# Kernel optimization log

Measured on AMD Instinct MI355X. Metric: run time of the kernel, lower is better.

Reference implementation:

```python
import jax, jax.numpy as jnp
import numpy as np

D_MODEL = 256
N_HEADS = 8
D_FFN = 1024
B, N = 4, 1024
HEAD_DIM = D_MODEL // N_HEADS
LN_EPS = 1e-5


def _ln(x, g, b):
    mu = jnp.mean(x, axis=-1, keepdims=True)
    var = jnp.var(x, axis=-1, keepdims=True)
    return (x - mu) * jax.lax.rsqrt(var + LN_EPS) * g + b


def setup_inputs() -> dict:
    key = jax.random.key(0)
    ks = jax.random.split(key, 16)
    s = 0.02
    return {
        "embed": jax.random.normal(ks[0], (B, N, D_MODEL), jnp.float32),
        "refer_bbox": jax.random.uniform(ks[1], (B, N, 4), jnp.float32),
        "dist": jax.random.uniform(ks[2], (B, N, N), jnp.float32),
        "query_pos": jax.random.normal(ks[3], (B, N, D_MODEL), jnp.float32),
        "in_proj_w": jax.random.normal(ks[4], (3 * D_MODEL, D_MODEL), jnp.float32) * s,
        "in_proj_b": jnp.zeros((3 * D_MODEL,), jnp.float32),
        "out_w": jax.random.normal(ks[5], (D_MODEL, D_MODEL), jnp.float32) * s,
        "out_b": jnp.zeros((D_MODEL,), jnp.float32),
        "tau_w": jax.random.normal(ks[6], (N_HEADS, D_MODEL), jnp.float32) * s,
        "tau_b": jax.random.uniform(ks[7], (N_HEADS,), jnp.float32, 0.0, 2.0),
        "w1": jax.random.normal(ks[8], (D_FFN, D_MODEL), jnp.float32) * s,
        "b1": jnp.zeros((D_FFN,), jnp.float32),
        "w2": jax.random.normal(ks[9], (D_MODEL, D_FFN), jnp.float32) * s,
        "b2": jnp.zeros((D_MODEL,), jnp.float32),
        "g1": jnp.ones((D_MODEL,), jnp.float32),
        "beta1": jnp.zeros((D_MODEL,), jnp.float32),
        "g2": jnp.ones((D_MODEL,), jnp.float32),
        "beta2": jnp.zeros((D_MODEL,), jnp.float32),
    }


def reference(embed, refer_bbox, dist, query_pos, in_proj_w, in_proj_b, out_w, out_b,
              tau_w, tau_b, w1, b1, w2, b2, g1, beta1, g2, beta2):
    # tau: (B, N, H) -> (B, H, N); additive bias mask[b,h,i,j] = dist[b,i,j] * tau[b,h,i]
    tau = (embed @ tau_w.T + tau_b).transpose(0, 2, 1)
    bias = dist[:, None, :, :] * tau[..., None]  # (B, H, N, N)

    qk = embed + query_pos  # q = k = embed + pos, v = embed
    wq, wk, wv = jnp.split(in_proj_w, 3, axis=0)
    bq, bk, bv = jnp.split(in_proj_b, 3, axis=0)
    q = (qk @ wq.T + bq).reshape(B, N, N_HEADS, HEAD_DIM)
    k = (qk @ wk.T + bk).reshape(B, N, N_HEADS, HEAD_DIM)
    v = (embed @ wv.T + bv).reshape(B, N, N_HEADS, HEAD_DIM)

    scores = jnp.einsum("bihd,bjhd->bhij", q, k) / np.sqrt(HEAD_DIM) + bias
    attn = jax.nn.softmax(scores, axis=-1)
    ctx = jnp.einsum("bhij,bjhd->bihd", attn, v).reshape(B, N, D_MODEL)
    tgt = ctx @ out_w.T + out_b

    x = _ln(embed + tgt, g1, beta1)
    ffn = jax.nn.relu(x @ w1.T + b1) @ w2.T + b2
    return _ln(x + ffn, g2, beta2)
```

## Files before the change

### kernel.cpp

```cpp
#include <hip/hip_runtime.h>
#include <math.h>

#define D_MODEL 256
#define N_HEADS 8
#define HEAD_DIM 32
#define D_FFN   1024
#define BB      4
#define NN      1024
#define M_TOT   (BB * NN)
#define LN_EPS  1e-5f

#define QSCALE_LOG2E 0.2550348612f
#define LOG2E        1.4426950408889634f

typedef float f32x4 __attribute__((ext_vector_type(4)));
typedef short bf16x8 __attribute__((ext_vector_type(8)));

__device__ __forceinline__ unsigned short f2bf(float f) {
    unsigned int u = __float_as_uint(f);
    unsigned int r = (u + 0x7fffu + ((u >> 16) & 1u)) >> 16;
    return (unsigned short)r;
}
__device__ __forceinline__ ushort4 pack4(float4 v) {
    ushort4 o; o.x = f2bf(v.x); o.y = f2bf(v.y); o.z = f2bf(v.z); o.w = f2bf(v.w);
    return o;
}
__device__ __forceinline__ float fast_exp2(float x) {
#if __has_builtin(__builtin_amdgcn_exp2f)
    return __builtin_amdgcn_exp2f(x);
#else
    return exp2f(x);
#endif
}

__global__ __launch_bounds__(256)
void prep_all_kernel(const float4* __restrict__ e, const float4* __restrict__ qp,
                     ushort4* __restrict__ ebf, ushort4* __restrict__ qkbf,
                     const float4* __restrict__ inw, const float4* __restrict__ outw,
                     const float4* __restrict__ w1, const float4* __restrict__ w2,
                     const float4* __restrict__ tauw,
                     ushort4* __restrict__ o_inw, ushort4* __restrict__ o_outw,
                     ushort4* __restrict__ o_w1, ushort4* __restrict__ o_w2,
                     ushort4* __restrict__ o_taupad) {
    if (blockIdx.x < 1024) {
        int i = blockIdx.x * 256 + threadIdx.x;
        float4 ev = e[i], pv = qp[i];
        ebf[i] = pack4(ev);
        float4 s = make_float4(ev.x + pv.x, ev.y + pv.y, ev.z + pv.z, ev.w + pv.w);
        qkbf[i] = pack4(s);
    } else {
        int i = (blockIdx.x - 1024) * 256 + threadIdx.x;
        if (i < 49152)       o_inw[i] = pack4(inw[i]);
        else if (i < 65536)  o_outw[i - 49152] = pack4(outw[i - 49152]);
        else if (i < 131072) o_w1[i - 65536] = pack4(w1[i - 65536]);
        else if (i < 196608) o_w2[i - 131072] = pack4(w2[i - 131072]);
        else if (i < 200704) {
            int q = i - 196608;
            if (q < 512) o_taupad[q] = pack4(tauw[q]);
            else { ushort4 z = {0, 0, 0, 0}; o_taupad[q] = z; }
        }
    }
}

__global__ __launch_bounds__(256)
void qkv_mfma_kernel(const unsigned short* __restrict__ qk_bf,
                     const unsigned short* __restrict__ emb_bf,
                     const unsigned short* __restrict__ inw_bf,
                     const unsigned short* __restrict__ taupad,
                     const float* __restrict__ in_proj_b, const float* __restrict__ tau_b,
                     unsigned short* __restrict__ qb, unsigned short* __restrict__ kb,
                     unsigned short* __restrict__ vbT, float* __restrict__ taub) {
    const int w    = threadIdx.x >> 6;
    const int lane = threadIdx.x & 63;
    const int l16 = lane & 15, l4 = lane >> 4;
    const int n0 = blockIdx.x * 64;
    const int m0 = blockIdx.y * 64;
    const int wm = (w >> 1) * 32, wn = (w & 1) * 32;

    const unsigned short* A = (blockIdx.x < 8) ? qk_bf : emb_bf;
    const unsigned short* W0 = (n0 < 768) ? &inw_bf[(size_t)(n0 + wn + l16) * D_MODEL]
                                          : &taupad[(size_t)(wn + l16) * D_MODEL];
    const unsigned short* Ar0 = &A[(size_t)(m0 + wm + l16) * D_MODEL];

    f32x4 acc[2][2] = {};
    #pragma unroll
    for (int k0 = 0; k0 < D_MODEL; k0 += 32) {
        bf16x8 a0 = *(const bf16x8*)&Ar0[k0 + l4 * 8];
        bf16x8 a1 = *(const bf16x8*)&Ar0[16 * D_MODEL + k0 + l4 * 8];
        bf16x8 b0 = *(const bf16x8*)&W0[k0 + l4 * 8];
        bf16x8 b1 = *(const bf16x8*)&W0[16 * D_MODEL + k0 + l4 * 8];
        acc[0][0] = __builtin_amdgcn_mfma_f32_16x16x32_bf16(a0, b0, acc[0][0], 0, 0, 0);
        acc[0][1] = __builtin_amdgcn_mfma_f32_16x16x32_bf16(a0, b1, acc[0][1], 0, 0, 0);
        acc[1][0] = __builtin_amdgcn_mfma_f32_16x16x32_bf16(a1, b0, acc[1][0], 0, 0, 0);
        acc[1][1] = __builtin_amdgcn_mfma_f32_16x16x32_bf16(a1, b1, acc[1][1], 0, 0, 0);
    }

    #pragma unroll
    for (int i = 0; i < 2; i++) {
        #pragma unroll
        for (int j = 0; j < 2; j++) {
            #pragma unroll
            for (int r = 0; r < 4; r++) {
                const int m = m0 + wm + i * 16 + l4 * 4 + r;
                const int b = m >> 10, nrow = m & 1023;
                const int c = n0 + wn + j * 16 + l16;
                float v = acc[i][j][r];
                if (c < 256) {
                    v = (v + in_proj_b[c]) * QSCALE_LOG2E;
                    int h = c >> 5, d = c & 31;
                    qb[((size_t)(b * N_HEADS + h) * NN + nrow) * HEAD_DIM + d] = f2bf(v);
                } else if (c < 512) {
                    v += in_proj_b[c];
                    int cc = c - 256; int h = cc >> 5, d = cc & 31;
                    kb[((size_t)(b * N_HEADS + h) * NN + nrow) * HEAD_DIM + d] = f2bf(v);
                } else if (c < 768) {
                    v += in_proj_b[c];
                    int cc = c - 512; int h = cc >> 5, d = cc & 31;
                    vbT[((size_t)(b * N_HEADS + h) * HEAD_DIM + d) * NN + nrow] = f2bf(v);
                } else if (c < 776) {
                    v = (v + tau_b[c - 768]) * LOG2E;
                    taub[(size_t)(b * N_HEADS + (c - 768)) * NN + nrow] = v;
                }
            }
        }
    }
}

__global__ __launch_bounds__(256)
void attn_mfma_kernel(const unsigned short* __restrict__ qb,
                      const unsigned short* __restrict__ kb,
                      const unsigned short* __restrict__ vbT,
                      const float* __restrict__ taub,
                      const float* __restrict__ dist,
                      float* __restrict__ Opart,
                      float* __restrict__ lpart) {
    __shared__ unsigned short Plds[4][16 * 72];
    const int w    = threadIdx.x >> 6;
    const int lane = threadIdx.x & 63;
    const int l16  = lane & 15;
    const int l4   = lane >> 4;
    const int bh = blockIdx.y;
    const int b = bh >> 3;
    const int z = blockIdx.z;
    const int i0 = blockIdx.x * 64 + w * 16;
    const int jbase = z * 256;

    const f32x4 zero = {0.f, 0.f, 0.f, 0.f};
    bf16x8 qf = *(const bf16x8*)&qb[((size_t)bh * NN + i0 + l16) * HEAD_DIM + l4 * 8];

    float tau_r[4];
    const float* drow[4];
    #pragma unroll
    for (int r = 0; r < 4; r++) {
        tau_r[r] = taub[(size_t)bh * NN + i0 + l4 * 4 + r];
        drow[r] = &dist[((size_t)b * NN + i0 + l4 * 4 + r) * NN];
    }

    float l_acc[4] = {0.f, 0.f, 0.f, 0.f};
    f32x4 O0 = zero, O1 = zero;

    unsigned short* pw = &Plds[w][0];
    const unsigned short* kbase = &kb[(size_t)bh * NN * HEAD_DIM];
    const unsigned short* vbase = &vbT[(size_t)bh * HEAD_DIM * NN];

    bf16x8 kf[4];
    float dd[4][4];
    #pragma unroll
    for (int s = 0; s < 4; s++)
        kf[s] = *(const bf16x8*)&kbase[(size_t)(jbase + s * 16 + l16) * HEAD_DIM + l4 * 8];
    #pragma unroll
    for (int s = 0; s < 4; s++)
        #pragma unroll
        for (int r = 0; r < 4; r++)
            dd[s][r] = drow[r][jbase + s * 16 + l16];

    for (int kt = 0; kt < 4; kt++) {
        const int j0 = jbase + kt * 64;
        bf16x8 vf[2][2];
        #pragma unroll
        for (int c = 0; c < 2; c++) {
            vf[c][0] = *(const bf16x8*)&vbase[(size_t)l16 * NN + j0 + c * 32 + l4 * 8];
            vf[c][1] = *(const bf16x8*)&vbase[(size_t)(16 + l16) * NN + j0 + c * 32 + l4 * 8];
        }
        bf16x8 kf_n[4];
        float dd_n[4][4];
        if (kt < 3) {
            const int j1 = j0 + 64;
            #pragma unroll
            for (int s = 0; s < 4; s++)
                kf_n[s] = *(const bf16x8*)&kbase[(size_t)(j1 + s * 16 + l16) * HEAD_DIM + l4 * 8];
            #pragma unroll
            for (int s = 0; s < 4; s++)
                #pragma unroll
                for (int r = 0; r < 4; r++)
                    dd_n[s][r] = drow[r][j1 + s * 16 + l16];
        }

        float parr[4][4];
        #pragma unroll
        for (int s = 0; s < 4; s++) {
            f32x4 S = __builtin_amdgcn_mfma_f32_16x16x32_bf16(qf, kf[s], zero, 0, 0, 0);
            #pragma unroll
            for (int r = 0; r < 4; r++) {
                const float p = fast_exp2(S[r] + dd[s][r] * tau_r[r]);
                parr[s][r] = p;
                l_acc[r] += p;
            }
        }

        #pragma unroll
        for (int s = 0; s < 4; s++)
            #pragma unroll
            for (int r = 0; r < 4; r++)
                pw[(l4 * 4 + r) * 72 + s * 16 + l16] = f2bf(parr[s][r]);
        asm volatile("s_waitcnt lgkmcnt(0)" ::: "memory");
        #pragma unroll
        for (int c = 0; c < 2; c++) {
            bf16x8 pf = *(const bf16x8*)&pw[l16 * 72 + c * 32 + l4 * 8];
            O0 = __builtin_amdgcn_mfma_f32_16x16x32_bf16(pf, vf[c][0], O0, 0, 0, 0);
            O1 = __builtin_amdgcn_mfma_f32_16x16x32_bf16(pf, vf[c][1], O1, 0, 0, 0);
        }

        if (kt < 3) {
            #pragma unroll
            for (int s = 0; s < 4; s++) {
                kf[s] = kf_n[s];
                #pragma unroll
                for (int r = 0; r < 4; r++) dd[s][r] = dd_n[s][r];
            }
        }
    }

    #pragma unroll
    for (int msk = 1; msk < 16; msk <<= 1)
        #pragma unroll
        for (int r = 0; r < 4; r++)
            l_acc[r] += __shfl_xor(l_acc[r], msk, 16);

    #pragma unroll
    for (int r = 0; r < 4; r++) {
        const int i = i0 + l4 * 4 + r;
        float* crow = &Opart[((size_t)(z * 32 + bh) * NN + i) * 32];
        crow[l16]      = O0[r];
        crow[16 + l16] = O1[r];
        if (l16 == 0)
            lpart[(size_t)(z * 32 + bh) * NN + i] = l_acc[r];
    }
}

__global__ __launch_bounds__(1024)
void post_kernel(const float* __restrict__ Opart, const float* __restrict__ lpart,
                 const unsigned short* __restrict__ outw,
                 const float* __restrict__ out_b, const float* __restrict__ embed,
                 const float* __restrict__ g1, const float* __restrict__ beta1,
                 const unsigned short* __restrict__ w1, const float* __restrict__ b1,
                 const unsigned short* __restrict__ w2, const float* __restrict__ b2,
                 const float* __restrict__ g2, const float* __restrict__ beta2,
                 float* __restrict__ out) {
    __shared__ float Lh[16][8];
    __shared__ unsigned short cs[16][264];
    __shared__ unsigned short xs[16][264];
    __shared__ unsigned short fs[16][1032];
    __shared__ float sums[16][4][4][2];

    const int tid = threadIdx.x;
    const int w = tid >> 6, lane = tid & 63;
    const int l16 = lane & 15, l4 = lane >> 4;
    const int m0 = blockIdx.x * 16;
    const int b = m0 >> 10;

    if (tid < 128) {
        const int row = tid >> 3, h = tid & 7;
        const int i = (m0 + row) & 1023;
        const int rowA = ((b * 8 + h) << 10) + i;
        float l = 0.f;
        #pragma unroll
        for (int z = 0; z < 4; z++) l += lpart[z * 32768 + rowA];
        Lh[row][h] = 1.0f / l;
    }
    __syncthreads();

    if (tid < 512) {
        const int row = tid >> 5;
        const int d0 = (tid & 31) * 8;
        const int h = d0 >> 5;
        const int dd = d0 & 31;
        const int i = (m0 + row) & 1023;
        const int rowA = ((b * 8 + h) << 10) + i;
        f32x4 s0 = {0.f, 0.f, 0.f, 0.f}, s1 = {0.f, 0.f, 0.f, 0.f};
        #pragma unroll
        for (int z = 0; z < 4; z++) {
            const float* u = &Opart[((size_t)(z * 32768 + rowA)) * 32 + dd];
            s0 += *(const f32x4*)u;
            s1 += *(const f32x4*)(u + 4);
        }
        const float li = Lh[row][h];
        #pragma unroll
        for (int j = 0; j < 4; j++) {
            cs[row][d0 + j]     = f2bf(s0[j] * li);
            cs[row][d0 + 4 + j] = f2bf(s1[j] * li);
        }
    }
    __syncthreads();

    const int cA = w * 16 + l16;
    f32x4 a0 = {}, a1 = {};
    {
        const unsigned short* wr = &outw[(size_t)cA * D_MODEL];
        #pragma unroll
        for (int kk = 0; kk < 4; kk++) {
            const int k0 = kk * 32, k1 = 128 + kk * 32;
            bf16x8 x0 = *(const bf16x8*)&cs[l16][k0 + l4 * 8];
            bf16x8 b0 = *(const bf16x8*)&wr[k0 + l4 * 8];
            bf16x8 x1 = *(const bf16x8*)&cs[l16][k1 + l4 * 8];
            bf16x8 b1v = *(const bf16x8*)&wr[k1 + l4 * 8];
            a0 = __builtin_amdgcn_mfma_f32_16x16x32_bf16(x0, b0, a0, 0, 0, 0);
            a1 = __builtin_amdgcn_mfma_f32_16x16x32_bf16(x1, b1v, a1, 0, 0, 0);
        }
    }
    float xv[4];
    {
        float s_r[4] = {0.f, 0.f, 0.f, 0.f}, q_r[4] = {0.f, 0.f, 0.f, 0.f};
        const float bs = out_b[cA];
        #pragma unroll
        for (int r = 0; r < 4; r++) {
            const int m = m0 + l4 * 4 + r;
            const float t = a0[r] + a1[r] + bs + embed[(size_t)m * D_MODEL + cA];
            xv[r] = t; s_r[r] += t; q_r[r] += t * t;
        }
        #pragma unroll
        for (int msk = 1; msk < 16; msk <<= 1)
            #pragma unroll
            for (int r = 0; r < 4; r++) {
                s_r[r] += __shfl_xor(s_r[r], msk, 16);
                q_r[r] += __shfl_xor(q_r[r], msk, 16);
            }
        if (l16 == 0)
            #pragma unroll
            for (int r = 0; r < 4; r++) {
                sums[w][l4][r][0] = s_r[r];
                sums[w][l4][r][1] = q_r[r];
            }
    }
    __syncthreads();
    #pragma unroll
    for (int r = 0; r < 4; r++) {
        float s = 0.f, q = 0.f;
        #pragma unroll
        for (int ww = 0; ww < 16; ww++) { s += sums[ww][l4][r][0]; q += sums[ww][l4][r][1]; }
        const float mu = s * (1.0f / D_MODEL);
        const float var = q * (1.0f / D_MODEL) - mu * mu;
        const float rstd = rsqrtf(var + LN_EPS);
        const float ov = (xv[r] - mu) * rstd * g1[cA] + beta1[cA];
        xv[r] = ov;
        xs[l4 * 4 + r][cA] = f2bf(ov);
    }
    __syncthreads();

    f32x4 accB[4] = {};
    #pragma unroll
    for (int k0 = 0; k0 < D_MODEL; k0 += 32) {
        bf16x8 a = *(const bf16x8*)&xs[l16][k0 + l4 * 8];
        #pragma unroll
        for (int j = 0; j < 4; j++) {
            const int fc = w * 64 + j * 16 + l16;
            bf16x8 bj = *(const bf16x8*)&w1[(size_t)fc * D_MODEL + k0 + l4 * 8];
            accB[j] = __builtin_amdgcn_mfma_f32_16x16x32_bf16(a, bj, accB[j], 0, 0, 0);
        }
    }
    #pragma unroll
    for (int j = 0; j < 4; j++) {
        const int fc = w * 64 + j * 16 + l16;
        const float bs = b1[fc];
        #pragma unroll
        for (int r = 0; r < 4; r++)
            fs[l4 * 4 + r][fc] = f2bf(fmaxf(accB[j][r] + bs, 0.f));
    }
    __syncthreads();

    f32x4 c0 = {}, c1 = {};
    {
        const unsigned short* wr = &w2[(size_t)cA * D_FFN];
        #pragma unroll
        for (int kk = 0; kk < 16; kk++) {
            const int k0 = kk * 32, k1 = 512 + kk * 32;
            bf16x8 f0 = *(const bf16x8*)&fs[l16][k0 + l4 * 8];
            bf16x8 b0 = *(const bf16x8*)&wr[k0 + l4 * 8];
            bf16x8 f1 = *(const bf16x8*)&fs[l16][k1 + l4 * 8];
            bf16x8 b1v = *(const bf16x8*)&wr[k1 + l4 * 8];
            c0 = __builtin_amdgcn_mfma_f32_16x16x32_bf16(f0, b0, c0, 0, 0, 0);
            c1 = __builtin_amdgcn_mfma_f32_16x16x32_bf16(f1, b1v, c1, 0, 0, 0);
        }
    }
    float v2[4];
    {
        float s_r[4] = {0.f, 0.f, 0.f, 0.f}, q_r[4] = {0.f, 0.f, 0.f, 0.f};
        const float bs = b2[cA];
        #pragma unroll
        for (int r = 0; r < 4; r++) {
            const float t = c0[r] + c1[r] + bs + xv[r];
            v2[r] = t; s_r[r] += t; q_r[r] += t * t;
        }
        #pragma unroll
        for (int msk = 1; msk < 16; msk <<= 1)
            #pragma unroll
            for (int r = 0; r < 4; r++) {
                s_r[r] += __shfl_xor(s_r[r], msk, 16);
                q_r[r] += __shfl_xor(q_r[r], msk, 16);
            }
        if (l16 == 0)
            #pragma unroll
            for (int r = 0; r < 4; r++) {
                sums[w][l4][r][0] = s_r[r];
                sums[w][l4][r][1] = q_r[r];
            }
    }
    __syncthreads();
    #pragma unroll
    for (int r = 0; r < 4; r++) {
        float s = 0.f, q = 0.f;
        #pragma unroll
        for (int ww = 0; ww < 16; ww++) { s += sums[ww][l4][r][0]; q += sums[ww][l4][r][1]; }
        const float mu = s * (1.0f / D_MODEL);
        const float var = q * (1.0f / D_MODEL) - mu * mu;
        const float rstd = rsqrtf(var + LN_EPS);
        const int m = m0 + l4 * 4 + r;
        out[(size_t)m * D_MODEL + cA] = (v2[r] - mu) * rstd * g2[cA] + beta2[cA];
    }
}

extern "C" void kernel_launch(void* const* d_in, const int* in_sizes, int n_in,
                              void* d_out, int out_size, void* d_ws, size_t ws_size,
                              hipStream_t stream) {
    const float* embed     = (const float*)d_in[0];
    const float* dist      = (const float*)d_in[2];
    const float* query_pos = (const float*)d_in[3];
    const float* in_proj_w = (const float*)d_in[4];
    const float* in_proj_b = (const float*)d_in[5];
    const float* out_w     = (const float*)d_in[6];
    const float* out_b     = (const float*)d_in[7];
    const float* tau_w     = (const float*)d_in[8];
    const float* tau_b     = (const float*)d_in[9];
    const float* w1        = (const float*)d_in[10];
    const float* b1        = (const float*)d_in[11];
    const float* w2        = (const float*)d_in[12];
    const float* b2        = (const float*)d_in[13];
    const float* g1        = (const float*)d_in[14];
    const float* beta1     = (const float*)d_in[15];
    const float* g2        = (const float*)d_in[16];
    const float* beta2     = (const float*)d_in[17];
    float* out = (float*)d_out;

    char* ws = (char*)d_ws;
    const size_t MB = 1024 * 1024;
    const size_t KB = 1024;
    unsigned short* emb_bf  = (unsigned short*)(ws);
    unsigned short* qk_bf   = (unsigned short*)(ws + 2 * MB);
    unsigned short* qb      = (unsigned short*)(ws + 4 * MB);
    unsigned short* kb      = (unsigned short*)(ws + 6 * MB);
    unsigned short* vbT     = (unsigned short*)(ws + 8 * MB);
    float*          taub    = (float*)(ws + 10 * MB);
    unsigned short* inw_bf  = (unsigned short*)(ws + 11 * MB);
    unsigned short* outw_bf = (unsigned short*)(ws + 11 * MB + 512 * KB);
    unsigned short* w1_bf   = (unsigned short*)(ws + 12 * MB);
    unsigned short* w2_bf   = (unsigned short*)(ws + 12 * MB + 512 * KB);
    unsigned short* taupad  = (unsigned short*)(ws + 13 * MB);
    float*          Opart   = (float*)(ws + 14 * MB);
    float*          lpart   = (float*)(ws + 30 * MB);

    prep_all_kernel<<<dim3(1808), dim3(256), 0, stream>>>(
        (const float4*)embed, (const float4*)query_pos,
        (ushort4*)emb_bf, (ushort4*)qk_bf,
        (const float4*)in_proj_w, (const float4*)out_w, (const float4*)w1,
        (const float4*)w2, (const float4*)tau_w,
        (ushort4*)inw_bf, (ushort4*)outw_bf, (ushort4*)w1_bf, (ushort4*)w2_bf,
        (ushort4*)taupad);

    qkv_mfma_kernel<<<dim3(13, M_TOT / 64), dim3(256), 0, stream>>>(
        qk_bf, emb_bf, inw_bf, taupad, in_proj_b, tau_b, qb, kb, vbT, taub);

    attn_mfma_kernel<<<dim3(NN / 64, BB * N_HEADS, 4), dim3(256), 0, stream>>>(
        qb, kb, vbT, taub, dist, Opart, lpart);

    post_kernel<<<dim3(M_TOT / 16), dim3(1024), 0, stream>>>(
        Opart, lpart, outw_bf, out_b, embed, g1, beta1,
        w1_bf, b1, w2_bf, b2, g2, beta2, out);
}
```

Before: 191.9 us.

## Stage K/V in LDS, vectorize dist loads, store partials in bf16, prefetch FFN weights

The attention kernel now copies each block's K and V fragments into shared memory once, shared by all four waves, instead of each wave loading them from global memory with register prefetch. It also permutes key columns so dist can be read as float4 per row. Attention partial outputs are written as bf16 rather than fp32, which halves the traffic between the attention and post kernels at some cost in precision. The post kernel adds software prefetch of the w1 and w2 weight fragments in the FFN GEMM loops.

```diff
diff --git a/kernel.cpp b/kernel.cpp
--- a/kernel.cpp
+++ b/kernel.cpp
@@ -31,6 +31,9 @@
 #else
     return exp2f(x);
 #endif
+}
+__device__ __forceinline__ float bf2f(unsigned short s) {
+    return __uint_as_float(((unsigned int)s) << 16);
 }
 
 __global__ __launch_bounds__(256)
@@ -132,8 +135,10 @@
                       const unsigned short* __restrict__ vbT,
                       const float* __restrict__ taub,
                       const float* __restrict__ dist,
-                      float* __restrict__ Opart,
+                      unsigned short* __restrict__ Opart,
                       float* __restrict__ lpart) {
+    __shared__ unsigned short Kf[4][4][512];
+    __shared__ unsigned short Vf[4][2][2][512];
     __shared__ unsigned short Plds[4][16 * 72];
     const int w    = threadIdx.x >> 6;
     const int lane = threadIdx.x & 63;
@@ -145,89 +150,74 @@
     const int i0 = blockIdx.x * 64 + w * 16;
     const int jbase = z * 256;
 
+    {
+        const int kt = w;
+        const unsigned short* kb_z = &kb[((size_t)bh * NN + jbase + kt * 64) * HEAD_DIM];
+        #pragma unroll
+        for (int s = 0; s < 4; s++) {
+            bf16x8 kv = *(const bf16x8*)&kb_z[(size_t)(l16 * 4 + s) * HEAD_DIM + l4 * 8];
+            *(bf16x8*)&Kf[kt][s][lane * 8] = kv;
+        }
+        const unsigned short* vb_z = &vbT[(size_t)bh * HEAD_DIM * NN + jbase + kt * 64];
+        #pragma unroll
+        for (int c = 0; c < 2; c++)
+            #pragma unroll
+            for (int h2 = 0; h2 < 2; h2++) {
+                bf16x8 vv = *(const bf16x8*)&vb_z[(size_t)(h2 * 16 + l16) * NN + c * 32 + l4 * 8];
+                *(bf16x8*)&Vf[kt][c][h2][lane * 8] = vv;
+            }
+    }
+
     const f32x4 zero = {0.f, 0.f, 0.f, 0.f};
     bf16x8 qf = *(const bf16x8*)&qb[((size_t)bh * NN + i0 + l16) * HEAD_DIM + l4 * 8];
-
     float tau_r[4];
     const float* drow[4];
     #pragma unroll
     for (int r = 0; r < 4; r++) {
         tau_r[r] = taub[(size_t)bh * NN + i0 + l4 * 4 + r];
-        drow[r] = &dist[((size_t)b * NN + i0 + l4 * 4 + r) * NN];
-    }
-
+        drow[r] = &dist[((size_t)b * NN + i0 + l4 * 4 + r) * NN + jbase];
+    }
     float l_acc[4] = {0.f, 0.f, 0.f, 0.f};
     f32x4 O0 = zero, O1 = zero;
-
     unsigned short* pw = &Plds[w][0];
-    const unsigned short* kbase = &kb[(size_t)bh * NN * HEAD_DIM];
-    const unsigned short* vbase = &vbT[(size_t)bh * HEAD_DIM * NN];
-
-    bf16x8 kf[4];
-    float dd[4][4];
-    #pragma unroll
-    for (int s = 0; s < 4; s++)
-        kf[s] = *(const bf16x8*)&kbase[(size_t)(jbase + s * 16 + l16) * HEAD_DIM + l4 * 8];
-    #pragma unroll
-    for (int s = 0; s < 4; s++)
+
+    __syncthreads();
+
+    for (int kt = 0; kt < 4; kt++) {
+        const int j0 = kt * 64;
+        f32x4 dd4[4];
         #pragma unroll
         for (int r = 0; r < 4; r++)
-            dd[s][r] = drow[r][jbase + s * 16 + l16];
-
-    for (int kt = 0; kt < 4; kt++) {
-        const int j0 = jbase + kt * 64;
-        bf16x8 vf[2][2];
-        #pragma unroll
-        for (int c = 0; c < 2; c++) {
-            vf[c][0] = *(const bf16x8*)&vbase[(size_t)l16 * NN + j0 + c * 32 + l4 * 8];
-            vf[c][1] = *(const bf16x8*)&vbase[(size_t)(16 + l16) * NN + j0 + c * 32 + l4 * 8];
-        }
-        bf16x8 kf_n[4];
-        float dd_n[4][4];
-        if (kt < 3) {
-            const int j1 = j0 + 64;
-            #pragma unroll
-            for (int s = 0; s < 4; s++)
-                kf_n[s] = *(const bf16x8*)&kbase[(size_t)(j1 + s * 16 + l16) * HEAD_DIM + l4 * 8];
-            #pragma unroll
-            for (int s = 0; s < 4; s++)
-                #pragma unroll
-                for (int r = 0; r < 4; r++)
-                    dd_n[s][r] = drow[r][j1 + s * 16 + l16];
-        }
+            dd4[r] = *(const f32x4*)&drow[r][j0 + l16 * 4];
 
         float parr[4][4];
         #pragma unroll
         for (int s = 0; s < 4; s++) {
-            f32x4 S = __builtin_amdgcn_mfma_f32_16x16x32_bf16(qf, kf[s], zero, 0, 0, 0);
-            #pragma unroll
-            for (int r = 0; r < 4; r++) {
-                const float p = fast_exp2(S[r] + dd[s][r] * tau_r[r]);
+            bf16x8 kfr = *(const bf16x8*)&Kf[kt][s][lane * 8];
+            f32x4 S = __builtin_amdgcn_mfma_f32_16x16x32_bf16(qf, kfr, zero, 0, 0, 0);
+            #pragma unroll
+            for (int r = 0; r < 4; r++) {
+                const float p = fast_exp2(S[r] + dd4[r][s] * tau_r[r]);
                 parr[s][r] = p;
                 l_acc[r] += p;
             }
         }
 
         #pragma unroll
-        for (int s = 0; s < 4; s++)
-            #pragma unroll
-            for (int r = 0; r < 4; r++)
-                pw[(l4 * 4 + r) * 72 + s * 16 + l16] = f2bf(parr[s][r]);
+        for (int r = 0; r < 4; r++) {
+            ushort4 pk;
+            pk.x = f2bf(parr[0][r]); pk.y = f2bf(parr[1][r]);
+            pk.z = f2bf(parr[2][r]); pk.w = f2bf(parr[3][r]);
+            *(ushort4*)&pw[(l4 * 4 + r) * 72 + l16 * 4] = pk;
+        }
         asm volatile("s_waitcnt lgkmcnt(0)" ::: "memory");
         #pragma unroll
         for (int c = 0; c < 2; c++) {
             bf16x8 pf = *(const bf16x8*)&pw[l16 * 72 + c * 32 + l4 * 8];
-            O0 = __builtin_amdgcn_mfma_f32_16x16x32_bf16(pf, vf[c][0], O0, 0, 0, 0);
-            O1 = __builtin_amdgcn_mfma_f32_16x16x32_bf16(pf, vf[c][1], O1, 0, 0, 0);
-        }
-
-        if (kt < 3) {
-            #pragma unroll
-            for (int s = 0; s < 4; s++) {
-                kf[s] = kf_n[s];
-                #pragma unroll
-                for (int r = 0; r < 4; r++) dd[s][r] = dd_n[s][r];
-            }
+            bf16x8 v0 = *(const bf16x8*)&Vf[kt][c][0][lane * 8];
+            bf16x8 v1 = *(const bf16x8*)&Vf[kt][c][1][lane * 8];
+            O0 = __builtin_amdgcn_mfma_f32_16x16x32_bf16(pf, v0, O0, 0, 0, 0);
+            O1 = __builtin_amdgcn_mfma_f32_16x16x32_bf16(pf, v1, O1, 0, 0, 0);
         }
     }
 
@@ -240,16 +230,16 @@
     #pragma unroll
     for (int r = 0; r < 4; r++) {
         const int i = i0 + l4 * 4 + r;
-        float* crow = &Opart[((size_t)(z * 32 + bh) * NN + i) * 32];
-        crow[l16]      = O0[r];
-        crow[16 + l16] = O1[r];
+        unsigned short* crow = &Opart[((size_t)(z * 32 + bh) * NN + i) * 32];
+        crow[l16]      = f2bf(O0[r]);
+        crow[16 + l16] = f2bf(O1[r]);
         if (l16 == 0)
             lpart[(size_t)(z * 32 + bh) * NN + i] = l_acc[r];
     }
 }
 
 __global__ __launch_bounds__(1024)
-void post_kernel(const float* __restrict__ Opart, const float* __restrict__ lpart,
+void post_kernel(const unsigned short* __restrict__ Opart, const float* __restrict__ lpart,
                  const unsigned short* __restrict__ outw,
                  const float* __restrict__ out_b, const float* __restrict__ embed,
                  const float* __restrict__ g1, const float* __restrict__ beta1,
@@ -287,19 +277,17 @@
         const int dd = d0 & 31;
         const int i = (m0 + row) & 1023;
         const int rowA = ((b * 8 + h) << 10) + i;
-        f32x4 s0 = {0.f, 0.f, 0.f, 0.f}, s1 = {0.f, 0.f, 0.f, 0.f};
+        float s[8] = {};
         #pragma unroll
         for (int z = 0; z < 4; z++) {
-            const float* u = &Opart[((size_t)(z * 32768 + rowA)) * 32 + dd];
-            s0 += *(const f32x4*)u;
-            s1 += *(const f32x4*)(u + 4);
+            bf16x8 u = *(const bf16x8*)&Opart[((size_t)(z * 32768 + rowA)) * 32 + dd];
+            #pragma unroll
+            for (int j = 0; j < 8; j++) s[j] += bf2f((unsigned short)u[j]);
         }
         const float li = Lh[row][h];
         #pragma unroll
-        for (int j = 0; j < 4; j++) {
-            cs[row][d0 + j]     = f2bf(s0[j] * li);
-            cs[row][d0 + 4 + j] = f2bf(s1[j] * li);
-        }
+        for (int j = 0; j < 8; j++)
+            cs[row][d0 + j] = f2bf(s[j] * li);
     }
     __syncthreads();
 
@@ -358,14 +346,27 @@
     __syncthreads();
 
     f32x4 accB[4] = {};
-    #pragma unroll
-    for (int k0 = 0; k0 < D_MODEL; k0 += 32) {
-        bf16x8 a = *(const bf16x8*)&xs[l16][k0 + l4 * 8];
-        #pragma unroll
-        for (int j = 0; j < 4; j++) {
-            const int fc = w * 64 + j * 16 + l16;
-            bf16x8 bj = *(const bf16x8*)&w1[(size_t)fc * D_MODEL + k0 + l4 * 8];
-            accB[j] = __builtin_amdgcn_mfma_f32_16x16x32_bf16(a, bj, accB[j], 0, 0, 0);
+    {
+        bf16x8 wf[4], wfn[4];
+        #pragma unroll
+        for (int j = 0; j < 4; j++)
+            wf[j] = *(const bf16x8*)&w1[(size_t)(w * 64 + j * 16 + l16) * D_MODEL + l4 * 8];
+        #pragma unroll
+        for (int kk = 0; kk < 8; kk++) {
+            const int k0 = kk * 32;
+            if (kk < 7) {
+                #pragma unroll
+                for (int j = 0; j < 4; j++)
+                    wfn[j] = *(const bf16x8*)&w1[(size_t)(w * 64 + j * 16 + l16) * D_MODEL + k0 + 32 + l4 * 8];
+            }
+            bf16x8 a = *(const bf16x8*)&xs[l16][k0 + l4 * 8];
+            #pragma unroll
+            for (int j = 0; j < 4; j++)
+                accB[j] = __builtin_amdgcn_mfma_f32_16x16x32_bf16(a, wf[j], accB[j], 0, 0, 0);
+            if (kk < 7) {
+                #pragma unroll
+                for (int j = 0; j < 4; j++) wf[j] = wfn[j];
+            }
         }
     }
     #pragma unroll
@@ -381,15 +382,20 @@
     f32x4 c0 = {}, c1 = {};
     {
         const unsigned short* wr = &w2[(size_t)cA * D_FFN];
+        bf16x8 wb0 = *(const bf16x8*)&wr[l4 * 8];
+        bf16x8 wb1 = *(const bf16x8*)&wr[512 + l4 * 8];
         #pragma unroll
         for (int kk = 0; kk < 16; kk++) {
             const int k0 = kk * 32, k1 = 512 + kk * 32;
+            bf16x8 cur0 = wb0, cur1 = wb1;
+            if (kk < 15) {
+                wb0 = *(const bf16x8*)&wr[k0 + 32 + l4 * 8];
+                wb1 = *(const bf16x8*)&wr[k1 + 32 + l4 * 8];
+            }
             bf16x8 f0 = *(const bf16x8*)&fs[l16][k0 + l4 * 8];
-            bf16x8 b0 = *(const bf16x8*)&wr[k0 + l4 * 8];
             bf16x8 f1 = *(const bf16x8*)&fs[l16][k1 + l4 * 8];
-            bf16x8 b1v = *(const bf16x8*)&wr[k1 + l4 * 8];
-            c0 = __builtin_amdgcn_mfma_f32_16x16x32_bf16(f0, b0, c0, 0, 0, 0);
-            c1 = __builtin_amdgcn_mfma_f32_16x16x32_bf16(f1, b1v, c1, 0, 0, 0);
+            c0 = __builtin_amdgcn_mfma_f32_16x16x32_bf16(f0, cur0, c0, 0, 0, 0);
+            c1 = __builtin_amdgcn_mfma_f32_16x16x32_bf16(f1, cur1, c1, 0, 0, 0);
         }
     }
     float v2[4];
@@ -465,8 +471,8 @@
     unsigned short* w1_bf   = (unsigned short*)(ws + 12 * MB);
     unsigned short* w2_bf   = (unsigned short*)(ws + 12 * MB + 512 * KB);
     unsigned short* taupad  = (unsigned short*)(ws + 13 * MB);
-    float*          Opart   = (float*)(ws + 14 * MB);
-    float*          lpart   = (float*)(ws + 30 * MB);
+    unsigned short* Opart   = (unsigned short*)(ws + 14 * MB);
+    float*          lpart   = (float*)(ws + 22 * MB);
 
     prep_all_kernel<<<dim3(1808), dim3(256), 0, stream>>>(
         (const float4*)embed, (const float4*)query_pos,
```

Result: faster. 180.8 us (-5.8%).
